# Performance work log

Measured on AMD Instinct MI355X. Metric: run time of the kernel, lower is better.

The kernel has to match this reference:

```python
import jax, jax.numpy as jnp
import numpy as np

B, N, M = 2, 4096, 4096
DQ = DKV = DOUT = 512
HEADS, DH = 8, 64
INNER = HEADS * DH
SCALE = DH ** -0.5


def _ln(x, g, b, eps=1e-5):
    mu = jnp.mean(x, axis=-1, keepdims=True)
    var = jnp.mean(jnp.square(x - mu), axis=-1, keepdims=True)
    return (x - mu) * jax.lax.rsqrt(var + eps) * g + b


def setup_inputs() -> dict:
    key = jax.random.key(0)
    ks = jax.random.split(key, 12)
    s = lambda fan: 1.0 / np.sqrt(fan)
    return {
        "q0": jax.random.normal(ks[0], (B, N, DQ), jnp.float32),
        "kv0": jax.random.normal(ks[1], (B, M, DKV), jnp.float32),
        "normq_g": jnp.ones((DQ,), jnp.float32),
        "normq_b": jnp.zeros((DQ,), jnp.float32),
        "normkv_g": jnp.ones((DKV,), jnp.float32),
        "normkv_b": jnp.zeros((DKV,), jnp.float32),
        "Wq": jax.random.normal(ks[2], (DQ, INNER), jnp.float32) * s(DQ),
        "Wk": jax.random.normal(ks[3], (DKV, INNER), jnp.float32) * s(DKV),
        "Wv": jax.random.normal(ks[4], (DKV, INNER), jnp.float32) * s(DKV),
        "Wr": jax.random.normal(ks[5], (INNER, DQ), jnp.float32) * s(INNER),
        "mlp_g": jnp.ones((DQ,), jnp.float32),
        "mlp_b": jnp.zeros((DQ,), jnp.float32),
        "W1": jax.random.normal(ks[6], (DQ, DOUT), jnp.float32) * s(DQ),
        "b1": jnp.zeros((DOUT,), jnp.float32),
        "W2": jax.random.normal(ks[7], (DOUT, DOUT), jnp.float32) * s(DOUT),
        "b2": jnp.zeros((DOUT,), jnp.float32),
    }


def reference(q0, kv0, normq_g, normq_b, normkv_g, normkv_b,
              Wq, Wk, Wv, Wr, mlp_g, mlp_b, W1, b1, W2, b2):
    # projections
    q = _ln(q0, normq_g, normq_b) @ Wq                    # [B,N,INNER]
    kv = _ln(kv0, normkv_g, normkv_b)                     # [B,M,DKV]
    k = kv @ Wk                                           # [B,M,INNER]
    v = kv @ Wv                                           # [B,M,INNER]
    # split heads: b n (h d) -> b h n d
    q = q.reshape(B, N, HEADS, DH).transpose(0, 2, 1, 3)
    k = k.reshape(B, M, HEADS, DH).transpose(0, 2, 1, 3)
    v = v.reshape(B, M, HEADS, DH).transpose(0, 2, 1, 3)
    dots = jnp.einsum('bhnd,bhmd->bhnm', q, k) * SCALE    # [B,H,N,M]
    attn = jax.nn.softmax(dots, axis=-1)
    out = jnp.einsum('bhnm,bhmd->bhnd', attn, v)          # [B,H,N,DH]
    out = out.transpose(0, 2, 1, 3).reshape(B, N, INNER)  # b h n d -> b n (h d)
    out = out @ Wr + q0                                   # [B,N,DQ]
    # MLP branch with residual
    h = _ln(out, mlp_g, mlp_b)
    h = jax.nn.relu(h @ W1 + b1) @ W2 + b2
    return out + h
```

## Files before the change

kernel.cpp:

```cpp
#include <hip/hip_runtime.h>

typedef unsigned short u16;
typedef unsigned int u32;
typedef __bf16 bf16x8 __attribute__((ext_vector_type(8)));
typedef float f32x4 __attribute__((ext_vector_type(4)));
typedef u16 u16x8 __attribute__((ext_vector_type(8)));

#define SC2 0.18033688011112042f

__device__ __forceinline__ u16 bf16rne(float f) {
  u32 u = __float_as_uint(f);
  u32 r = (u + 0x7FFFu + ((u >> 16) & 1u)) >> 16;
  return (u16)r;
}
__device__ __forceinline__ u32 packrne(float a, float b) {
  return (u32)bf16rne(a) | ((u32)bf16rne(b) << 16);
}
__device__ __forceinline__ float b2f(u16 v) {
  return __uint_as_float(((u32)v) << 16);
}

__device__ __forceinline__ void async16(const void* g, void* l) {
  __builtin_amdgcn_global_load_lds(
      (__attribute__((address_space(1))) void*)(g),
      (__attribute__((address_space(3))) void*)(l), 16, 0, 0);
}
template <int N>
__device__ __forceinline__ void vm_wait() {
  asm volatile("s_waitcnt vmcnt(%0)" ::"n"(N) : "memory");
}
__device__ __forceinline__ void lgkm_wait0() {
  asm volatile("s_waitcnt lgkmcnt(0)" ::: "memory");
}
__device__ __forceinline__ void bar() {
  asm volatile("s_barrier" ::: "memory");
}

__global__ __launch_bounds__(256) void wtrans_kernel(
    const float* __restrict__ w0, const float* __restrict__ w1,
    const float* __restrict__ w2, const float* __restrict__ w3,
    const float* __restrict__ w4, const float* __restrict__ w5,
    u16* __restrict__ out) {
  __shared__ u16 T[64 * 72];
  int t = threadIdx.x;
  int widx = blockIdx.y;
  int k0 = (blockIdx.x & 7) * 64, n0 = (blockIdx.x >> 3) * 64;
  const float* W = w0;
  if (widx == 1) W = w1; else if (widx == 2) W = w2; else if (widx == 3) W = w3;
  else if (widx == 4) W = w4; else if (widx == 5) W = w5;
#pragma unroll
  for (int p = 0; p < 4; ++p) {
    int kr = p * 16 + (t >> 4);
    int nc = (t & 15) * 4;
    float4 v = *(const float4*)(W + (size_t)(k0 + kr) * 512 + n0 + nc);
    T[(nc + 0) * 72 + kr] = bf16rne(v.x);
    T[(nc + 1) * 72 + kr] = bf16rne(v.y);
    T[(nc + 2) * 72 + kr] = bf16rne(v.z);
    T[(nc + 3) * 72 + kr] = bf16rne(v.w);
  }
  __syncthreads();
  u16* ob = out + (size_t)widx * 262144;
#pragma unroll
  for (int p = 0; p < 2; ++p) {
    int idx = p * 256 + t;
    int nr = idx >> 3, ch = idx & 7;
    uint4 val = *(const uint4*)(T + nr * 72 + ch * 8);
    *(uint4*)(ob + (size_t)(n0 + nr) * 512 + k0 + ch * 8) = val;
  }
}

__device__ __forceinline__ void ln_row(const float* xr, const float* gp,
                                       const float* bp, u16* orow, int lane) {
  const float* xl = xr + lane * 8;
  float4 a0 = *(const float4*)xl;
  float4 a1 = *(const float4*)(xl + 4);
  float v[8] = {a0.x, a0.y, a0.z, a0.w, a1.x, a1.y, a1.z, a1.w};
  float s = 0.f, s2 = 0.f;
#pragma unroll
  for (int j = 0; j < 8; ++j) { s += v[j]; s2 += v[j] * v[j]; }
#pragma unroll
  for (int off = 32; off; off >>= 1) {
    s += __shfl_xor(s, off);
    s2 += __shfl_xor(s2, off);
  }
  float mu = s * (1.0f / 512.0f);
  float rstd = rsqrtf(s2 * (1.0f / 512.0f) - mu * mu + 1e-5f);
  const float* gl = gp + lane * 8;
  const float* bl = bp + lane * 8;
  float4 g0 = *(const float4*)gl, g1 = *(const float4*)(gl + 4);
  float4 b0 = *(const float4*)bl, b1 = *(const float4*)(bl + 4);
  float gg[8] = {g0.x, g0.y, g0.z, g0.w, g1.x, g1.y, g1.z, g1.w};
  float bb[8] = {b0.x, b0.y, b0.z, b0.w, b1.x, b1.y, b1.z, b1.w};
  u16x8 ov;
#pragma unroll
  for (int j = 0; j < 8; ++j) ov[j] = bf16rne((v[j] - mu) * rstd * gg[j] + bb[j]);
  *(u16x8*)(orow + lane * 8) = ov;
}

__global__ __launch_bounds__(256) void ln_kernel(
    const float* __restrict__ x, const float* __restrict__ g,
    const float* __restrict__ b, u16* __restrict__ o) {
  int w = threadIdx.x >> 6, lane = threadIdx.x & 63;
  size_t row = (size_t)blockIdx.x * 4 + w;
  ln_row(x + row * 512, g, b, o + row * 512, lane);
}

__global__ __launch_bounds__(256) void ln2_kernel(
    const float* __restrict__ x0, const float* __restrict__ g0,
    const float* __restrict__ b0, u16* __restrict__ o0,
    const float* __restrict__ x1, const float* __restrict__ g1,
    const float* __restrict__ b1, u16* __restrict__ o1) {
  int w = threadIdx.x >> 6, lane = threadIdx.x & 63;
  size_t row = (size_t)blockIdx.x * 4 + w;
  if (row < 8192) {
    ln_row(x0 + row * 512, g0, b0, o0 + row * 512, lane);
  } else {
    size_t r2 = row - 8192;
    ln_row(x1 + r2 * 512, g1, b1, o1 + r2 * 512, lane);
  }
}

template <int MODE>
__global__ __launch_bounds__(256) void gemm512_kernel(
    const u16* __restrict__ A, const u16* __restrict__ Bt, void* __restrict__ Cv,
    void* __restrict__ Cv2, const float* __restrict__ bias,
    const float* __restrict__ res) {
  __shared__ __align__(16) u16 As[2][4096];
  __shared__ __align__(16) u16 Bs[2][2048];
  const int t = threadIdx.x;
  const int lane = t & 63;
  const int w = t >> 6;
  const int row0 = blockIdx.y * 128;
  const int col0 = blockIdx.x * 64;
  f32x4 acc[2][4];
#pragma unroll
  for (int i = 0; i < 2; ++i)
#pragma unroll
    for (int j = 0; j < 4; ++j) acc[i][j] = (f32x4){0.f, 0.f, 0.f, 0.f};

#define GSTAGE(buf, k0)                                                          \
  {                                                                              \
    _Pragma("unroll") for (int i = 0; i < 2; ++i) {                              \
      int s = t + 256 * i;                                                       \
      int mts = s >> 6, L = s & 63;                                              \
      async16(A + (size_t)(row0 + mts * 16 + (L & 15)) * 512 + (k0) + (L >> 4) * 8, \
              (char*)As[buf] + s * 16);                                          \
    }                                                                            \
    {                                                                            \
      int s = t;                                                                 \
      int nts = s >> 6, L = s & 63;                                              \
      async16(Bt + (size_t)(col0 + nts * 16 + (L & 15)) * 512 + (k0) + (L >> 4) * 8, \
              (char*)Bs[buf] + s * 16);                                          \
    }                                                                            \
  }

  GSTAGE(0, 0);

  for (int kk = 0; kk < 16; ++kk) {
    if (kk < 15) {
      GSTAGE((kk + 1) & 1, (kk + 1) * 32);
      vm_wait<3>();
    } else {
      vm_wait<0>();
    }
    bar();
    const u16* Ac = As[kk & 1];
    const u16* Bc = Bs[kk & 1];
    bf16x8 Af[2], Bf[4];
#pragma unroll
    for (int mt = 0; mt < 2; ++mt)
      Af[mt] = *(const bf16x8*)(Ac + ((w * 2 + mt) * 64 + lane) * 8);
#pragma unroll
    for (int nt = 0; nt < 4; ++nt)
      Bf[nt] = *(const bf16x8*)(Bc + (nt * 64 + lane) * 8);
#pragma unroll
    for (int mt = 0; mt < 2; ++mt)
#pragma unroll
      for (int nt = 0; nt < 4; ++nt)
        acc[mt][nt] = __builtin_amdgcn_mfma_f32_16x16x32_bf16(Af[mt], Bf[nt], acc[mt][nt], 0, 0, 0);
    bar();
  }

  const int q = lane >> 4, cl = lane & 15;
#pragma unroll
  for (int mt = 0; mt < 2; ++mt) {
#pragma unroll
    for (int nt = 0; nt < 4; ++nt) {
      int col = col0 + nt * 16 + cl;
      if (MODE == 6 && col >= 512) {
        int d = col - 512;
        int bb = row0 >> 12;
        int mloc = (row0 & 4095) + (w * 2 + mt) * 16 + q * 4;
        uint2 pk;
        pk.x = packrne(acc[mt][nt][0], acc[mt][nt][1]);
        pk.y = packrne(acc[mt][nt][2], acc[mt][nt][3]);
        *(uint2*)((u16*)Cv2 + ((size_t)bb * 512 + d) * 4096 + mloc) = pk;
        continue;
      }
#pragma unroll
      for (int r = 0; r < 4; ++r) {
        int row = row0 + (w * 2 + mt) * 16 + q * 4 + r;
        float v = acc[mt][nt][r];
        if (MODE == 0 || MODE == 6) {
          ((u16*)Cv)[(size_t)row * 512 + col] = bf16rne(v);
        } else if (MODE == 1) {
          size_t idx = (size_t)row * 512 + col;
          ((float*)Cv)[idx] = v + res[idx];
        } else if (MODE == 2) {
          v += bias[col];
          ((u16*)Cv)[(size_t)row * 512 + col] = bf16rne(fmaxf(v, 0.f));
        } else if (MODE == 3) {
          size_t idx = (size_t)row * 512 + col;
          ((float*)Cv)[idx] = v + bias[col] + res[idx];
        } else if (MODE == 4) {
          ((u16*)Cv)[(size_t)row * 512 + col] = bf16rne(v * SC2);
        }
      }
    }
  }
}

__global__ __launch_bounds__(128, 2) void attn_kernel(
    const u16* __restrict__ Q, const u16* __restrict__ K,
    const u16* __restrict__ VT, u16* __restrict__ O0, u16* __restrict__ O1,
    float* __restrict__ lpart) {
  __shared__ __align__(16) u16 Ks[2][4096];
  __shared__ __align__(16) u16 Vs[2][4096];
  __shared__ __align__(16) u16 Ps[2][1024];
  const int t = threadIdx.x;
  const int lane = t & 63;
  const int w = t >> 6;
  const int g = lane >> 4, cl = lane & 15;
  const int qt = blockIdx.x, h = blockIdx.y;
  const int b = blockIdx.z >> 1, sp = blockIdx.z & 1;
  const u16* Qg = Q + ((size_t)(b * 4096 + qt * 128 + w * 64)) * 512 + h * 64;
  const u16* Kg = K + ((size_t)(b * 4096 + sp * 2048)) * 512 + h * 64;
  const u16* VTg = VT + ((size_t)(b * 512 + h * 64)) * 4096 + sp * 2048;
  u16* Ob = (sp ? O1 : O0) + (((size_t)(b * 8 + h) * 4096) + qt * 128 + w * 64) * 64;
  float* lb = lpart + ((size_t)((sp * 2 + b) * 8 + h)) * 4096 + qt * 128 + w * 64;
  char* Pw = (char*)Ps[w];

#pragma unroll
  for (int i = 0; i < 8; ++i) {
    async16(Qg + (size_t)((i >> 1) * 16 + cl) * 512 + (i & 1) * 32 + g * 8,
            (char*)Ks[w] + (i * 64 + lane) * 16);
  }
  vm_wait<0>();
  bf16x8 Qb[4][2];
#pragma unroll
  for (int nt = 0; nt < 4; ++nt)
#pragma unroll
    for (int ks = 0; ks < 2; ++ks)
      Qb[nt][ks] = *(const bf16x8*)((char*)Ks[w] + ((nt * 2 + ks) * 64 + lane) * 16);
  lgkm_wait0();
  bar();

#define STAGEKV(buf, m0)                                                          \
  {                                                                               \
    _Pragma("unroll") for (int i = 0; i < 4; ++i) {                               \
      int s = t + 128 * i; int c = s >> 6; int L = s & 63;                        \
      async16(Kg + (size_t)((m0) + (c >> 1) * 16 + (L & 15)) * 512 + (c & 1) * 32 + (L >> 4) * 8, \
              (char*)Ks[buf] + s * 16);                                           \
    }                                                                             \
    _Pragma("unroll") for (int i = 0; i < 4; ++i) {                               \
      int s = t + 128 * i; int c = s >> 6; int L = s & 63;                        \
      async16(VTg + (size_t)((c >> 1) * 16 + (L & 15)) * 4096 + (m0) + (c & 1) * 32 + (L >> 4) * 8, \
              (char*)Vs[buf] + s * 16);                                           \
    }                                                                             \
  }

  STAGEKV(0, 0);

  u16x8 ou;
#pragma unroll
  for (int j = 0; j < 8; ++j) ou[j] = 0x3F80;
  bf16x8 ones = __builtin_bit_cast(bf16x8, ou);

  f32x4 Oa[4][4], ls[4];
#pragma unroll
  for (int i = 0; i < 4; ++i) {
    ls[i] = (f32x4){0.f, 0.f, 0.f, 0.f};
#pragma unroll
    for (int j = 0; j < 4; ++j) Oa[i][j] = (f32x4){0.f, 0.f, 0.f, 0.f};
  }
  const int s7 = cl & 7;

  for (int it = 0; it < 32; ++it) {
    if (it < 31) {
      STAGEKV((it + 1) & 1, (it + 1) * 64);
      vm_wait<8>();
    } else {
      vm_wait<0>();
    }
    bar();
    const u16* Kc = Ks[it & 1];
    const u16* Vc = Vs[it & 1];
    bf16x8 Kf[4][2], Vf[4][2];
#pragma unroll
    for (int mt = 0; mt < 4; ++mt)
#pragma unroll
      for (int ks = 0; ks < 2; ++ks) {
        Kf[mt][ks] = *(const bf16x8*)((const char*)Kc + ((mt * 2 + ks) * 64 + lane) * 16);
        Vf[mt][ks] = *(const bf16x8*)((const char*)Vc + ((mt * 2 + ks) * 64 + lane) * 16);
      }

#pragma unroll
    for (int nt = 0; nt < 4; ++nt) {
      f32x4 St[4];
#pragma unroll
      for (int mt = 0; mt < 4; ++mt) St[mt] = (f32x4){0.f, 0.f, 0.f, 0.f};
#pragma unroll
      for (int ks = 0; ks < 2; ++ks)
#pragma unroll
        for (int mt = 0; mt < 4; ++mt)
          St[mt] = __builtin_amdgcn_mfma_f32_16x16x32_bf16(Kf[mt][ks], Qb[nt][ks], St[mt], 0, 0, 0);

#pragma unroll
      for (int mt = 0; mt < 4; ++mt) {
        float p0 = __builtin_amdgcn_exp2f(St[mt][0]);
        float p1 = __builtin_amdgcn_exp2f(St[mt][1]);
        float p2 = __builtin_amdgcn_exp2f(St[mt][2]);
        float p3 = __builtin_amdgcn_exp2f(St[mt][3]);
        uint2 pk;
        pk.x = __builtin_amdgcn_perm(__float_as_uint(p1), __float_as_uint(p0), 0x07060302u);
        pk.y = __builtin_amdgcn_perm(__float_as_uint(p3), __float_as_uint(p2), 0x07060302u);
        *(uint2*)(Pw + cl * 128 + (((mt * 2 + (g >> 1)) ^ s7) << 4) + ((g & 1) << 3)) = pk;
      }
      bf16x8 Pb[2];
#pragma unroll
      for (int ks = 0; ks < 2; ++ks)
        Pb[ks] = *(const bf16x8*)(Pw + cl * 128 + (((ks * 4 + g) ^ s7) << 4));
      ls[nt] = __builtin_amdgcn_mfma_f32_16x16x32_bf16(ones, Pb[0], ls[nt], 0, 0, 0);
      ls[nt] = __builtin_amdgcn_mfma_f32_16x16x32_bf16(ones, Pb[1], ls[nt], 0, 0, 0);
#pragma unroll
      for (int ks = 0; ks < 2; ++ks)
#pragma unroll
        for (int mtd = 0; mtd < 4; ++mtd)
          Oa[mtd][nt] = __builtin_amdgcn_mfma_f32_16x16x32_bf16(Vf[mtd][ks], Pb[ks], Oa[mtd][nt], 0, 0, 0);
    }
    bar();
  }

#pragma unroll
  for (int nt = 0; nt < 4; ++nt) {
    int q = nt * 16 + cl;
#pragma unroll
    for (int mtd = 0; mtd < 4; ++mtd) {
      uint2 pk;
      pk.x = packrne(Oa[mtd][nt][0], Oa[mtd][nt][1]);
      pk.y = packrne(Oa[mtd][nt][2], Oa[mtd][nt][3]);
      *(uint2*)(Ob + (size_t)q * 64 + mtd * 16 + g * 4) = pk;
    }
    if (g == 0) lb[q] = ls[nt][0];
  }
}

__global__ __launch_bounds__(256) void combine_kernel(
    const u16* __restrict__ O0, const u16* __restrict__ O1,
    const float* __restrict__ lp, u16* __restrict__ out) {
  int idx = blockIdx.x * 256 + threadIdx.x;
  int dc = idx & 7;
  int q = (idx >> 3) & 4095;
  int h = (idx >> 15) & 7;
  int b = idx >> 18;
  size_t po = (((size_t)(b * 8 + h) * 4096) + q) * 64 + dc * 8;
  u16x8 a = *(const u16x8*)(O0 + po);
  u16x8 c = *(const u16x8*)(O1 + po);
  float l0 = lp[((size_t)(b * 8 + h)) * 4096 + q];
  float l1 = lp[((size_t)(16 + b * 8 + h)) * 4096 + q];
  float inv = 1.0f / (l0 + l1);
  u16x8 o;
#pragma unroll
  for (int j = 0; j < 8; ++j) o[j] = bf16rne((b2f(a[j]) + b2f(c[j])) * inv);
  *(u16x8*)(out + ((size_t)(b * 4096 + q)) * 512 + h * 64 + dc * 8) = o;
}

extern "C" void kernel_launch(void* const* d_in, const int* in_sizes, int n_in,
                              void* d_out, int out_size, void* d_ws, size_t ws_size,
                              hipStream_t stream) {
  const float* q0 = (const float*)d_in[0];
  const float* kv0 = (const float*)d_in[1];
  const float* nq_g = (const float*)d_in[2];
  const float* nq_b = (const float*)d_in[3];
  const float* nkv_g = (const float*)d_in[4];
  const float* nkv_b = (const float*)d_in[5];
  const float* Wq = (const float*)d_in[6];
  const float* Wk = (const float*)d_in[7];
  const float* Wv = (const float*)d_in[8];
  const float* Wr = (const float*)d_in[9];
  const float* mlp_g = (const float*)d_in[10];
  const float* mlp_b = (const float*)d_in[11];
  const float* W1 = (const float*)d_in[12];
  const float* b1 = (const float*)d_in[13];
  const float* W2 = (const float*)d_in[14];
  const float* b2 = (const float*)d_in[15];
  float* out = (float*)d_out;

  char* ws = (char*)d_ws;
  float* ob = (float*)(ws + 0);
  u16* O1p = (u16*)(ws + 0);
  u16* Qp = (u16*)(ws + 16777216);
  u16* aout = (u16*)(ws + 16777216);
  u16* Kp = (u16*)(ws + 25165824);
  u16* h1 = (u16*)(ws + 25165824);
  u16* VTp = (u16*)(ws + 33554432);
  u16* kvn2 = (u16*)(ws + 33554432);
  u16* wb = (u16*)(ws + 41943040);
  float* lpart = (float*)(ws + 45088768);
  u16* qn = (u16*)(ws + 46137344);
  u16* O0p = (u16*)(ws + 46137344);
  u16* kvn = (u16*)(ws + 54525952);
  u16* wqT = wb;
  u16* wkT = wb + 262144;
  u16* wrT = wb + 786432;
  u16* w1T = wb + 1048576;
  u16* w2T = wb + 1310720;

  dim3 blk(256);
  wtrans_kernel<<<dim3(64, 6), blk, 0, stream>>>(Wq, Wk, Wv, Wr, W1, W2, wb);
  ln2_kernel<<<4096, blk, 0, stream>>>(q0, nq_g, nq_b, qn, kv0, nkv_g, nkv_b, kvn);
  gemm512_kernel<4><<<dim3(8, 64), blk, 0, stream>>>(qn, wqT, Qp, nullptr, nullptr, nullptr);
  gemm512_kernel<6><<<dim3(16, 64), blk, 0, stream>>>(kvn, wkT, Kp, VTp, nullptr, nullptr);
  attn_kernel<<<dim3(32, 8, 4), dim3(128), 0, stream>>>(Qp, Kp, VTp, O0p, O1p, lpart);
  combine_kernel<<<2048, blk, 0, stream>>>(O0p, O1p, lpart, aout);
  gemm512_kernel<1><<<dim3(8, 64), blk, 0, stream>>>(aout, wrT, ob, nullptr, nullptr, q0);
  ln_kernel<<<2048, blk, 0, stream>>>(ob, mlp_g, mlp_b, kvn2);
  gemm512_kernel<2><<<dim3(8, 64), blk, 0, stream>>>(kvn2, w1T, h1, nullptr, b1, nullptr);
  gemm512_kernel<3><<<dim3(8, 64), blk, 0, stream>>>(h1, w2T, out, nullptr, b2, ob);
}
```

Measured before the change: 294.7 us.

## Merge prep and projection launches, deepen GEMM pipeline to four stages

The weight transpose and the two input layernorms now run in one launch, and the Q and KV projection GEMMs run in one launch, which removes two kernel launches and lets the work overlap. The GEMM main loop moves from double buffering to a four-buffer ring with three stages prefetched, and it drops the trailing barrier per k-step. LDS use per GEMM block doubles, which may lower occupancy.

```diff
diff --git a/kernel.cpp b/kernel.cpp
--- a/kernel.cpp
+++ b/kernel.cpp
@@ -34,39 +34,6 @@
 }
 __device__ __forceinline__ void bar() {
   asm volatile("s_barrier" ::: "memory");
-}
-
-__global__ __launch_bounds__(256) void wtrans_kernel(
-    const float* __restrict__ w0, const float* __restrict__ w1,
-    const float* __restrict__ w2, const float* __restrict__ w3,
-    const float* __restrict__ w4, const float* __restrict__ w5,
-    u16* __restrict__ out) {
-  __shared__ u16 T[64 * 72];
-  int t = threadIdx.x;
-  int widx = blockIdx.y;
-  int k0 = (blockIdx.x & 7) * 64, n0 = (blockIdx.x >> 3) * 64;
-  const float* W = w0;
-  if (widx == 1) W = w1; else if (widx == 2) W = w2; else if (widx == 3) W = w3;
-  else if (widx == 4) W = w4; else if (widx == 5) W = w5;
-#pragma unroll
-  for (int p = 0; p < 4; ++p) {
-    int kr = p * 16 + (t >> 4);
-    int nc = (t & 15) * 4;
-    float4 v = *(const float4*)(W + (size_t)(k0 + kr) * 512 + n0 + nc);
-    T[(nc + 0) * 72 + kr] = bf16rne(v.x);
-    T[(nc + 1) * 72 + kr] = bf16rne(v.y);
-    T[(nc + 2) * 72 + kr] = bf16rne(v.z);
-    T[(nc + 3) * 72 + kr] = bf16rne(v.w);
-  }
-  __syncthreads();
-  u16* ob = out + (size_t)widx * 262144;
-#pragma unroll
-  for (int p = 0; p < 2; ++p) {
-    int idx = p * 256 + t;
-    int nr = idx >> 3, ch = idx & 7;
-    uint4 val = *(const uint4*)(T + nr * 72 + ch * 8);
-    *(uint4*)(ob + (size_t)(n0 + nr) * 512 + k0 + ch * 8) = val;
-  }
 }
 
 __device__ __forceinline__ void ln_row(const float* xr, const float* gp,
@@ -97,6 +64,55 @@
   *(u16x8*)(orow + lane * 8) = ov;
 }
 
+__global__ __launch_bounds__(256) void prep_kernel(
+    const float* __restrict__ w0, const float* __restrict__ w1,
+    const float* __restrict__ w2, const float* __restrict__ w3,
+    const float* __restrict__ w4, const float* __restrict__ w5,
+    u16* __restrict__ wout,
+    const float* __restrict__ x0, const float* __restrict__ g0,
+    const float* __restrict__ b0, u16* __restrict__ o0,
+    const float* __restrict__ x1, const float* __restrict__ g1,
+    const float* __restrict__ b1, u16* __restrict__ o1) {
+  __shared__ u16 T[64 * 72];
+  int t = threadIdx.x;
+  int bx = blockIdx.x;
+  if (bx < 384) {
+    int widx = bx >> 6, tile = bx & 63;
+    int k0 = (tile & 7) * 64, n0 = (tile >> 3) * 64;
+    const float* W = w0;
+    if (widx == 1) W = w1; else if (widx == 2) W = w2; else if (widx == 3) W = w3;
+    else if (widx == 4) W = w4; else if (widx == 5) W = w5;
+#pragma unroll
+    for (int p = 0; p < 4; ++p) {
+      int kr = p * 16 + (t >> 4);
+      int nc = (t & 15) * 4;
+      float4 v = *(const float4*)(W + (size_t)(k0 + kr) * 512 + n0 + nc);
+      T[(nc + 0) * 72 + kr] = bf16rne(v.x);
+      T[(nc + 1) * 72 + kr] = bf16rne(v.y);
+      T[(nc + 2) * 72 + kr] = bf16rne(v.z);
+      T[(nc + 3) * 72 + kr] = bf16rne(v.w);
+    }
+    __syncthreads();
+    u16* ob = wout + (size_t)widx * 262144;
+#pragma unroll
+    for (int p = 0; p < 2; ++p) {
+      int idx = p * 256 + t;
+      int nr = idx >> 3, ch = idx & 7;
+      uint4 val = *(const uint4*)(T + nr * 72 + ch * 8);
+      *(uint4*)(ob + (size_t)(n0 + nr) * 512 + k0 + ch * 8) = val;
+    }
+  } else {
+    int w = t >> 6, lane = t & 63;
+    size_t row = (size_t)(bx - 384) * 4 + w;
+    if (row < 8192) {
+      ln_row(x0 + row * 512, g0, b0, o0 + row * 512, lane);
+    } else {
+      size_t r2 = row - 8192;
+      ln_row(x1 + r2 * 512, g1, b1, o1 + r2 * 512, lane);
+    }
+  }
+}
+
 __global__ __launch_bounds__(256) void ln_kernel(
     const float* __restrict__ x, const float* __restrict__ g,
     const float* __restrict__ b, u16* __restrict__ o) {
@@ -105,28 +121,51 @@
   ln_row(x + row * 512, g, b, o + row * 512, lane);
 }
 
-__global__ __launch_bounds__(256) void ln2_kernel(
-    const float* __restrict__ x0, const float* __restrict__ g0,
-    const float* __restrict__ b0, u16* __restrict__ o0,
-    const float* __restrict__ x1, const float* __restrict__ g1,
-    const float* __restrict__ b1, u16* __restrict__ o1) {
-  int w = threadIdx.x >> 6, lane = threadIdx.x & 63;
-  size_t row = (size_t)blockIdx.x * 4 + w;
-  if (row < 8192) {
-    ln_row(x0 + row * 512, g0, b0, o0 + row * 512, lane);
-  } else {
-    size_t r2 = row - 8192;
-    ln_row(x1 + r2 * 512, g1, b1, o1 + r2 * 512, lane);
-  }
-}
+#define GSTAGE(buf, k0)                                                          \
+  {                                                                              \
+    _Pragma("unroll") for (int i = 0; i < 2; ++i) {                              \
+      int s = t + 256 * i;                                                       \
+      int mts = s >> 6, L = s & 63;                                             \
+      async16(A + (size_t)(row0 + mts * 16 + (L & 15)) * 512 + (k0) + (L >> 4) * 8, \
+              (char*)As[buf] + s * 16);                                          \
+    }                                                                            \
+    {                                                                            \
+      int s = t;                                                                 \
+      int nts = s >> 6, L = s & 63;                                             \
+      async16(Bt + (size_t)(col0 + nts * 16 + (L & 15)) * 512 + (k0) + (L >> 4) * 8, \
+              (char*)Bs[buf] + s * 16);                                          \
+    }                                                                            \
+  }
+
+#define GEMM_CORE                                                                \
+  GSTAGE(0, 0);                                                                  \
+  GSTAGE(1, 32);                                                                 \
+  GSTAGE(2, 64);                                                                 \
+  _Pragma("unroll") for (int kk = 0; kk < 16; ++kk) {                            \
+    if (kk <= 13) vm_wait<6>();                                                  \
+    else if (kk == 14) vm_wait<3>();                                             \
+    else vm_wait<0>();                                                           \
+    bar();                                                                       \
+    if (kk < 13) GSTAGE((kk + 3) & 3, (kk + 3) * 32);                            \
+    const u16* Ac = As[kk & 3];                                                  \
+    const u16* Bc = Bs[kk & 3];                                                  \
+    bf16x8 Af[2], Bf[4];                                                         \
+    _Pragma("unroll") for (int mt = 0; mt < 2; ++mt)                             \
+        Af[mt] = *(const bf16x8*)(Ac + ((w * 2 + mt) * 64 + lane) * 8);          \
+    _Pragma("unroll") for (int nt = 0; nt < 4; ++nt)                             \
+        Bf[nt] = *(const bf16x8*)(Bc + (nt * 64 + lane) * 8);                    \
+    _Pragma("unroll") for (int mt = 0; mt < 2; ++mt)                             \
+        _Pragma("unroll") for (int nt = 0; nt < 4; ++nt)                         \
+            acc[mt][nt] = __builtin_amdgcn_mfma_f32_16x16x32_bf16(               \
+                Af[mt], Bf[nt], acc[mt][nt], 0, 0, 0);                           \
+  }
 
 template <int MODE>
 __global__ __launch_bounds__(256) void gemm512_kernel(
     const u16* __restrict__ A, const u16* __restrict__ Bt, void* __restrict__ Cv,
-    void* __restrict__ Cv2, const float* __restrict__ bias,
-    const float* __restrict__ res) {
-  __shared__ __align__(16) u16 As[2][4096];
-  __shared__ __align__(16) u16 Bs[2][2048];
+    const float* __restrict__ bias, const float* __restrict__ res) {
+  __shared__ __align__(16) u16 As[4][4096];
+  __shared__ __align__(16) u16 Bs[4][2048];
   const int t = threadIdx.x;
   const int lane = t & 63;
   const int w = t >> 6;
@@ -138,48 +177,7 @@
 #pragma unroll
     for (int j = 0; j < 4; ++j) acc[i][j] = (f32x4){0.f, 0.f, 0.f, 0.f};
 
-#define GSTAGE(buf, k0)                                                          \
-  {                                                                              \
-    _Pragma("unroll") for (int i = 0; i < 2; ++i) {                              \
-      int s = t + 256 * i;                                                       \
-      int mts = s >> 6, L = s & 63;                                              \
-      async16(A + (size_t)(row0 + mts * 16 + (L & 15)) * 512 + (k0) + (L >> 4) * 8, \
-              (char*)As[buf] + s * 16);                                          \
-    }                                                                            \
-    {                                                                            \
-      int s = t;                                                                 \
-      int nts = s >> 6, L = s & 63;                                              \
-      async16(Bt + (size_t)(col0 + nts * 16 + (L & 15)) * 512 + (k0) + (L >> 4) * 8, \
-              (char*)Bs[buf] + s * 16);                                          \
-    }                                                                            \
-  }
-
-  GSTAGE(0, 0);
-
-  for (int kk = 0; kk < 16; ++kk) {
-    if (kk < 15) {
-      GSTAGE((kk + 1) & 1, (kk + 1) * 32);
-      vm_wait<3>();
-    } else {
-      vm_wait<0>();
-    }
-    bar();
-    const u16* Ac = As[kk & 1];
-    const u16* Bc = Bs[kk & 1];
-    bf16x8 Af[2], Bf[4];
-#pragma unroll
-    for (int mt = 0; mt < 2; ++mt)
-      Af[mt] = *(const bf16x8*)(Ac + ((w * 2 + mt) * 64 + lane) * 8);
-#pragma unroll
-    for (int nt = 0; nt < 4; ++nt)
-      Bf[nt] = *(const bf16x8*)(Bc + (nt * 64 + lane) * 8);
-#pragma unroll
-    for (int mt = 0; mt < 2; ++mt)
-#pragma unroll
-      for (int nt = 0; nt < 4; ++nt)
-        acc[mt][nt] = __builtin_amdgcn_mfma_f32_16x16x32_bf16(Af[mt], Bf[nt], acc[mt][nt], 0, 0, 0);
-    bar();
-  }
+  GEMM_CORE
 
   const int q = lane >> 4, cl = lane & 15;
 #pragma unroll
@@ -187,33 +185,72 @@
 #pragma unroll
     for (int nt = 0; nt < 4; ++nt) {
       int col = col0 + nt * 16 + cl;
-      if (MODE == 6 && col >= 512) {
+#pragma unroll
+      for (int r = 0; r < 4; ++r) {
+        int row = row0 + (w * 2 + mt) * 16 + q * 4 + r;
+        float v = acc[mt][nt][r];
+        if (MODE == 1) {
+          size_t idx = (size_t)row * 512 + col;
+          ((float*)Cv)[idx] = v + res[idx];
+        } else if (MODE == 2) {
+          v += bias[col];
+          ((u16*)Cv)[(size_t)row * 512 + col] = bf16rne(fmaxf(v, 0.f));
+        } else {
+          size_t idx = (size_t)row * 512 + col;
+          ((float*)Cv)[idx] = v + bias[col] + res[idx];
+        }
+      }
+    }
+  }
+}
+
+__global__ __launch_bounds__(256) void proj_kernel(
+    const u16* __restrict__ Aq, const u16* __restrict__ BtQ, u16* __restrict__ Qp,
+    const u16* __restrict__ Akv, const u16* __restrict__ BtKV,
+    u16* __restrict__ Kp, u16* __restrict__ VTp) {
+  __shared__ __align__(16) u16 As[4][4096];
+  __shared__ __align__(16) u16 Bs[4][2048];
+  const int t = threadIdx.x;
+  const int lane = t & 63;
+  const int w = t >> 6;
+  const int bx = blockIdx.x;
+  const bool isq = bx < 8;
+  const u16* A = isq ? Aq : Akv;
+  const u16* Bt = isq ? BtQ : BtKV;
+  const int row0 = blockIdx.y * 128;
+  const int col0 = (isq ? bx : bx - 8) * 64;
+  f32x4 acc[2][4];
+#pragma unroll
+  for (int i = 0; i < 2; ++i)
+#pragma unroll
+    for (int j = 0; j < 4; ++j) acc[i][j] = (f32x4){0.f, 0.f, 0.f, 0.f};
+
+  GEMM_CORE
+
+  const int q = lane >> 4, cl = lane & 15;
+#pragma unroll
+  for (int mt = 0; mt < 2; ++mt) {
+#pragma unroll
+    for (int nt = 0; nt < 4; ++nt) {
+      int col = col0 + nt * 16 + cl;
+      if (!isq && col >= 512) {
         int d = col - 512;
         int bb = row0 >> 12;
         int mloc = (row0 & 4095) + (w * 2 + mt) * 16 + q * 4;
         uint2 pk;
         pk.x = packrne(acc[mt][nt][0], acc[mt][nt][1]);
         pk.y = packrne(acc[mt][nt][2], acc[mt][nt][3]);
-        *(uint2*)((u16*)Cv2 + ((size_t)bb * 512 + d) * 4096 + mloc) = pk;
+        *(uint2*)(VTp + ((size_t)bb * 512 + d) * 4096 + mloc) = pk;
         continue;
       }
 #pragma unroll
       for (int r = 0; r < 4; ++r) {
         int row = row0 + (w * 2 + mt) * 16 + q * 4 + r;
         float v = acc[mt][nt][r];
-        if (MODE == 0 || MODE == 6) {
-          ((u16*)Cv)[(size_t)row * 512 + col] = bf16rne(v);
-        } else if (MODE == 1) {
-          size_t idx = (size_t)row * 512 + col;
-          ((float*)Cv)[idx] = v + res[idx];
-        } else if (MODE == 2) {
-          v += bias[col];
-          ((u16*)Cv)[(size_t)row * 512 + col] = bf16rne(fmaxf(v, 0.f));
-        } else if (MODE == 3) {
-          size_t idx = (size_t)row * 512 + col;
-          ((float*)Cv)[idx] = v + bias[col] + res[idx];
-        } else if (MODE == 4) {
-          ((u16*)Cv)[(size_t)row * 512 + col] = bf16rne(v * SC2);
+        if (isq) {
+          Qp[(size_t)row * 512 + col] = bf16rne(v * SC2);
+        } else {
+          Kp[(size_t)row * 512 + col] = bf16rne(v);
         }
       }
     }
@@ -417,14 +454,13 @@
   u16* w2T = wb + 1310720;
 
   dim3 blk(256);
-  wtrans_kernel<<<dim3(64, 6), blk, 0, stream>>>(Wq, Wk, Wv, Wr, W1, W2, wb);
-  ln2_kernel<<<4096, blk, 0, stream>>>(q0, nq_g, nq_b, qn, kv0, nkv_g, nkv_b, kvn);
-  gemm512_kernel<4><<<dim3(8, 64), blk, 0, stream>>>(qn, wqT, Qp, nullptr, nullptr, nullptr);
-  gemm512_kernel<6><<<dim3(16, 64), blk, 0, stream>>>(kvn, wkT, Kp, VTp, nullptr, nullptr);
+  prep_kernel<<<4480, blk, 0, stream>>>(Wq, Wk, Wv, Wr, W1, W2, wb,
+                                        q0, nq_g, nq_b, qn, kv0, nkv_g, nkv_b, kvn);
+  proj_kernel<<<dim3(24, 64), blk, 0, stream>>>(qn, wqT, Qp, kvn, wkT, Kp, VTp);
   attn_kernel<<<dim3(32, 8, 4), dim3(128), 0, stream>>>(Qp, Kp, VTp, O0p, O1p, lpart);
   combine_kernel<<<2048, blk, 0, stream>>>(O0p, O1p, lpart, aout);
-  gemm512_kernel<1><<<dim3(8, 64), blk, 0, stream>>>(aout, wrT, ob, nullptr, nullptr, q0);
+  gemm512_kernel<1><<<dim3(8, 64), blk, 0, stream>>>(aout, wrT, ob, nullptr, q0);
   ln_kernel<<<2048, blk, 0, stream>>>(ob, mlp_g, mlp_b, kvn2);
-  gemm512_kernel<2><<<dim3(8, 64), blk, 0, stream>>>(kvn2, w1T, h1, nullptr, b1, nullptr);
-  gemm512_kernel<3><<<dim3(8, 64), blk, 0, stream>>>(h1, w2T, out, nullptr, b2, ob);
-}
+  gemm512_kernel<2><<<dim3(8, 64), blk, 0, stream>>>(kvn2, w1T, h1, b1, nullptr);
+  gemm512_kernel<3><<<dim3(8, 64), blk, 0, stream>>>(h1, w2T, out, b2, ob);
+}
```

After: 296.2 us. About the same (+0.5%).
